# Kernel optimization log

Measured on AMD Instinct MI355X. Metric: run time of the kernel, lower is better.

The kernel has to match this reference:

```python
import jax, jax.numpy as jnp
import numpy as np

G = 17  # groups == deform_groups
EPS = 1e-5

# regular 3x3 kernel grid in homogeneous coords: rows = (dy, dx, 1), cols = 9 kernel taps (row-major)
REG = jnp.array([[-1, -1, -1, 0, 0, 0, 1, 1, 1],
                 [-1, 0, 1, -1, 0, 1, -1, 0, 1],
                 [1, 1, 1, 1, 1, 1, 1, 1, 1]], dtype=jnp.float32)
KY = jnp.array([-1, -1, -1, 0, 0, 0, 1, 1, 1], dtype=jnp.float32)
KX = jnp.array([-1, 0, 1, -1, 0, 1, -1, 0, 1], dtype=jnp.float32)


def setup_inputs() -> dict:
    key = jax.random.key(0)
    k0, k1, k2 = jax.random.split(key, 3)
    B, C, H, W = 2, 272, 128, 128
    Cg = C // G
    x = jax.random.normal(k0, (B, C, H, W), jnp.float32)
    tm_w = jax.random.normal(k1, (6 * G, Cg, 3, 3), jnp.float32) * 0.02  # offset-transform conv weight
    tm_b = jnp.zeros((6 * G,), jnp.float32)
    dc_w = jax.random.normal(k2, (C, Cg, 3, 3), jnp.float32) * 0.05     # deform conv weight (no bias)
    gamma = jnp.ones((C,), jnp.float32)
    beta = jnp.zeros((C,), jnp.float32)
    return dict(x=x, tm_w=tm_w, tm_b=tm_b, dc_w=dc_w, gamma=gamma, beta=beta)


def _deform_sample(x, dy, dx):
    """Bilinear-sample x (B,C,H,W) at per-group offsets dy,dx (B,H,W,G,9).
    Returns (B,G,Cg,9,H,W). Zero padding outside the image (mmcv semantics)."""
    B, C, H, W = x.shape
    Cg = C // G
    hh = jnp.arange(H, dtype=x.dtype)[None, :, None, None, None]
    ww = jnp.arange(W, dtype=x.dtype)[None, None, :, None, None]
    py = hh + KY + dy  # (B,H,W,G,9)
    px = ww + KX + dx
    y0 = jnp.floor(py)
    x0 = jnp.floor(px)
    wy = py - y0
    wx = px - x0
    y0i = y0.astype(jnp.int32)
    x0i = x0.astype(jnp.int32)
    x_g = x.reshape(B, G, Cg, H * W)

    def corner(yi, xi, wgt):
        valid = (yi >= 0) & (yi < H) & (xi >= 0) & (xi < W)
        lin = jnp.clip(yi, 0, H - 1) * W + jnp.clip(xi, 0, W - 1)  # (B,H,W,G,9)
        lin = lin.transpose(0, 3, 4, 1, 2).reshape(B, G, 1, 9 * H * W)
        idx = jnp.broadcast_to(lin, (B, G, Cg, 9 * H * W))
        vals = jnp.take_along_axis(x_g, idx, axis=3).reshape(B, G, Cg, 9, H, W)
        w = (wgt * valid.astype(x.dtype)).transpose(0, 3, 4, 1, 2)  # (B,G,9,H,W)
        return vals * w[:, :, None]

    samp = corner(y0i, x0i, (1 - wy) * (1 - wx))
    samp = samp + corner(y0i, x0i + 1, (1 - wy) * wx)
    samp = samp + corner(y0i + 1, x0i, wy * (1 - wx))
    samp = samp + corner(y0i + 1, x0i + 1, wy * wx)
    return samp


def _forward(x, tm_w, tm_b, dc_w, gamma, beta):
    B, C, H, W = x.shape
    Cg = C // G
    # 1) offset-transform conv (grouped 3x3, SAME)
    aff = jax.lax.conv_general_dilated(
        x, tm_w, window_strides=(1, 1), padding='SAME',
        dimension_numbers=('NCHW', 'OIHW', 'NCHW'), feature_group_count=G)
    aff = aff + tm_b[None, :, None, None]  # (B,6G,H,W)
    # faithful to torch: view(B,2,3,G,H,W).permute(0,4,5,3,1,2) @ REG
    aff = aff.reshape(B, 2, 3, G, H, W).transpose(0, 4, 5, 3, 1, 2)  # (B,H,W,G,2,3)
    off = jnp.einsum('bhwgij,jk->bhwgik', aff, REG)  # (B,H,W,G,2,9)
    # DeformConv2d reads the flattened 18 channels as interleaved (dy,dx) pairs per tap
    off = off.reshape(B, H, W, G, 18).reshape(B, H, W, G, 9, 2)
    dy, dx = off[..., 0], off[..., 1]
    # 2) deformable 3x3 conv, groups=deform_groups=G, bias=False
    samp = _deform_sample(x, dy, dx)  # (B,G,Cg,9,H,W)
    w = dc_w.reshape(G, Cg, Cg, 3 * 3)  # (g, out-in-group, in-in-group, tap)
    out = jnp.einsum('bgckhw,gock->bgohw', samp, w).reshape(B, C, H, W)
    # 3) batch norm (training-mode stats) + residual ReLU
    mean = jnp.mean(out, axis=(0, 2, 3), keepdims=True)
    var = jnp.var(out, axis=(0, 2, 3), keepdims=True)
    out = (out - mean) * jax.lax.rsqrt(var + EPS)
    out = out * gamma[None, :, None, None] + beta[None, :, None, None]
    return jax.nn.relu(out + x)


def reference(x, tm_w, tm_b, dc_w, gamma, beta):
    return _forward(x, tm_w, tm_b, dc_w, gamma, beta)
```

## Files before the change

### kernel.cpp

```cpp
#include <hip/hip_runtime.h>
#include <math.h>

#define BB 2
#define CC 272
#define GG 17
#define CG 16
#define HH 128
#define WW 128
#define HWX (HH*WW)
#define AFFC 102
#define NSLAB (BB*GG)
#define TILES_PER_SLAB 64
#define NWG (NSLAB*TILES_PER_SLAB)
#define WGPX (NWG/8)

typedef float f4nt __attribute__((ext_vector_type(4)));
typedef unsigned u4nt __attribute__((ext_vector_type(4)));

__device__ __forceinline__ unsigned f2bf(float f) {
    unsigned u = __float_as_uint(f);
    return (u + 0x7fffu + ((u >> 16) & 1u)) >> 16;
}
__device__ __forceinline__ float bflo(unsigned u) { return __uint_as_float(u << 16); }
__device__ __forceinline__ float bfhi(unsigned u) { return __uint_as_float(u & 0xffff0000u); }

__global__ __launch_bounds__(256) void wt_kernel(
    const float* __restrict__ dc_w, const float* __restrict__ tm_w,
    float* __restrict__ dc_wt, float* __restrict__ tm_wt)
{
    int i = blockIdx.x * 256 + threadIdx.x;
    if (i < GG * CG * 9 * CG) {
        int oc = i & 15, t = (i >> 4) % 9, c = (i / 144) % 16, g = i / 2304;
        dc_wt[i] = dc_w[((size_t)(g * 16 + oc) * 16 + c) * 9 + t];
    }
    if (i < GG * 6 * 9 * CG) {
        int c = i & 15, t = (i >> 4) % 9, j = (i / 144) % 6, ig = i / 864;
        tm_wt[i] = tm_w[((size_t)(ig * 6 + j) * 16 + c) * 9 + t];
    }
}

__global__ __launch_bounds__(256) void transpose_kernel(
    const float* __restrict__ x, unsigned* __restrict__ xt)
{
    __shared__ float tile[CG][WW + 1];
    const int h = blockIdx.x & (HH - 1);
    const int g = (blockIdx.x >> 7) % GG;
    const int b = blockIdx.x / (GG * HH);
    const int tid = threadIdx.x;
    const float* src = x + (size_t)(b * CC + g * CG) * HWX + h * WW;
    for (int i = tid; i < CG * WW; i += 256) {
        int c = i >> 7, w = i & (WW - 1);
        tile[c][w] = src[(size_t)c * HWX + w];
    }
    __syncthreads();
    unsigned* dst = xt + ((size_t)(b * GG + g) * HWX + h * WW) * (CG / 2);
    for (int i = tid; i < CG * WW / 2; i += 256) {
        int w = i >> 3, c2 = i & 7;
        dst[i] = f2bf(tile[2 * c2][w]) | (f2bf(tile[2 * c2 + 1][w]) << 16);
    }
}

__global__ __launch_bounds__(256) void aff_conv_kernel(
    const unsigned* __restrict__ xt, const float* __restrict__ tm_wt,
    const float* __restrict__ tm_b, float* __restrict__ aff)
{
    const int ig = blockIdx.y;
    const int b = blockIdx.z;
    const int tid = threadIdx.x;

    const int p = blockIdx.x * 256 + tid;
    const int h = p >> 7, w = p & (WW - 1);
    const unsigned* xb = xt + (size_t)(b * GG + ig) * HWX * (CG / 2);
    const float* wb = tm_wt + (size_t)ig * (6 * 9 * CG);

    float acc[6];
#pragma unroll
    for (int j = 0; j < 6; ++j) acc[j] = 0.f;

#pragma unroll 1
    for (int t = 0; t < 9; ++t) {
        int hy = h + t / 3 - 1;
        int wx = w + t % 3 - 1;
        uint4 u0 = {0, 0, 0, 0}, u1 = {0, 0, 0, 0};
        if (hy >= 0 && hy < HH && wx >= 0 && wx < WW) {
            const uint4* px = (const uint4*)(xb + (size_t)(hy * WW + wx) * (CG / 2));
            u0 = px[0]; u1 = px[1];
        }
        float xv[16];
        xv[0] = bflo(u0.x);  xv[1] = bfhi(u0.x);  xv[2] = bflo(u0.y);  xv[3] = bfhi(u0.y);
        xv[4] = bflo(u0.z);  xv[5] = bfhi(u0.z);  xv[6] = bflo(u0.w);  xv[7] = bfhi(u0.w);
        xv[8] = bflo(u1.x);  xv[9] = bfhi(u1.x);  xv[10] = bflo(u1.y); xv[11] = bfhi(u1.y);
        xv[12] = bflo(u1.z); xv[13] = bfhi(u1.z); xv[14] = bflo(u1.w); xv[15] = bfhi(u1.w);
#pragma unroll
        for (int j = 0; j < 6; ++j) {
            const float* wp = wb + (j * 9 + t) * CG;
            float a = acc[j];
#pragma unroll
            for (int k = 0; k < 16; ++k) a = fmaf(xv[k], wp[k], a);
            acc[j] = a;
        }
    }
#pragma unroll
    for (int j = 0; j < 6; ++j)
        aff[(size_t)(b * AFFC + ig * 6 + j) * HWX + p] = acc[j] + tm_b[ig * 6 + j];
}


#define ACCE(T, CH, S) { \
    const float4* wp_ = (const float4*)(wg + ((CH) * 9 + (T)) * CG); \
    float4 q0 = wp_[0], q1 = wp_[1], q2 = wp_[2], q3 = wp_[3]; \
    acc[0]  = fmaf(S, q0.x, acc[0]);  acc[1]  = fmaf(S, q0.y, acc[1]); \
    acc[2]  = fmaf(S, q0.z, acc[2]);  acc[3]  = fmaf(S, q0.w, acc[3]); \
    acc[4]  = fmaf(S, q1.x, acc[4]);  acc[5]  = fmaf(S, q1.y, acc[5]); \
    acc[6]  = fmaf(S, q1.z, acc[6]);  acc[7]  = fmaf(S, q1.w, acc[7]); \
    acc[8]  = fmaf(S, q2.x, acc[8]);  acc[9]  = fmaf(S, q2.y, acc[9]); \
    acc[10] = fmaf(S, q2.z, acc[10]); acc[11] = fmaf(S, q2.w, acc[11]); \
    acc[12] = fmaf(S, q3.x, acc[12]); acc[13] = fmaf(S, q3.y, acc[13]); \
    acc[14] = fmaf(S, q3.z, acc[14]); acc[15] = fmaf(S, q3.w, acc[15]); }

#define SE2(UA, UB, UC, UD, CH, T) { \
    float sl = fmaf(w00, bflo(UA), fmaf(w01, bflo(UB), fmaf(w10, bflo(UC), w11 * bflo(UD)))); \
    float sh = fmaf(w00, bfhi(UA), fmaf(w01, bfhi(UB), fmaf(w10, bfhi(UC), w11 * bfhi(UD)))); \
    ACCE(T, (CH), sl) ACCE(T, (CH) + 1, sh) }

#define TAP(T, I0, K0, I1, K1) { \
    float dy = ((I0) ? a10 : a00) * (float)((K0) / 3 - 1) \
             + ((I0) ? a11 : a01) * (float)((K0) % 3 - 1) + ((I0) ? a12 : a02); \
    float dx = ((I1) ? a10 : a00) * (float)((K1) / 3 - 1) \
             + ((I1) ? a11 : a01) * (float)((K1) % 3 - 1) + ((I1) ? a12 : a02); \
    float py = (float)(h + (T) / 3 - 1) + dy; \
    float px = (float)(w + (T) % 3 - 1) + dx; \
    float y0f = floorf(py), x0f = floorf(px); \
    float wy = py - y0f, wx = px - x0f; \
    int y0 = (int)y0f, x0 = (int)x0f; \
    int y1 = y0 + 1, x1 = x0 + 1; \
    bool vy0 = (y0 >= 0) && (y0 < HH), vy1 = (y1 >= 0) && (y1 < HH); \
    bool vx0 = (x0 >= 0) && (x0 < WW), vx1 = (x1 >= 0) && (x1 < WW); \
    int y0c = min(max(y0, 0), HH - 1), y1c = min(max(y1, 0), HH - 1); \
    int x0c = min(max(x0, 0), WW - 1), x1c = min(max(x1, 0), WW - 1); \
    float w00 = (vy0 && vx0) ? (1.f - wy) * (1.f - wx) : 0.f; \
    float w01 = (vy0 && vx1) ? (1.f - wy) * wx : 0.f; \
    float w10 = (vy1 && vx0) ? wy * (1.f - wx) : 0.f; \
    float w11 = (vy1 && vx1) ? wy * wx : 0.f; \
    const uint4* pA = (const uint4*)(xb + (size_t)(y0c * WW + x0c) * (CG / 2)); \
    const uint4* pB = (const uint4*)(xb + (size_t)(y0c * WW + x1c) * (CG / 2)); \
    const uint4* pC = (const uint4*)(xb + (size_t)(y1c * WW + x0c) * (CG / 2)); \
    const uint4* pD = (const uint4*)(xb + (size_t)(y1c * WW + x1c) * (CG / 2)); \
    uint4 A0 = pA[0], A1 = pA[1], B0 = pB[0], B1 = pB[1]; \
    uint4 C0 = pC[0], C1 = pC[1], D0 = pD[0], D1 = pD[1]; \
    SE2(A0.x, B0.x, C0.x, D0.x, 0, T)  SE2(A0.y, B0.y, C0.y, D0.y, 2, T) \
    SE2(A0.z, B0.z, C0.z, D0.z, 4, T)  SE2(A0.w, B0.w, C0.w, D0.w, 6, T) \
    SE2(A1.x, B1.x, C1.x, D1.x, 8, T)  SE2(A1.y, B1.y, C1.y, D1.y, 10, T) \
    SE2(A1.z, B1.z, C1.z, D1.z, 12, T) SE2(A1.w, B1.w, C1.w, D1.w, 14, T) }

__global__ __launch_bounds__(256, 6) void deform_kernel(
    const unsigned* __restrict__ xt, const float* __restrict__ dc_wt,
    const float* __restrict__ aff_buf, unsigned* __restrict__ pre,
    float* __restrict__ stat_sum, float* __restrict__ stat_sqs)
{
    __shared__ float red[CG][4][2];

    const int bid = blockIdx.x;
    const int work = (bid & 7) * WGPX + (bid >> 3);
    const int slab = work / TILES_PER_SLAB;
    const int tile = work % TILES_PER_SLAB;
    const int b = slab / GG;
    const int g = slab % GG;

    const int tid = threadIdx.y * 16 + threadIdx.x;
    const int h = (tile >> 3) * 16 + threadIdx.y;
    const int w = (tile & 7) * 16 + threadIdx.x;

    const float* ab = aff_buf + (size_t)b * AFFC * HWX + h * WW + w;
    float a00 = __builtin_nontemporal_load(ab + (size_t)(0 * 51 + 0 * 17 + g) * HWX);
    float a01 = __builtin_nontemporal_load(ab + (size_t)(0 * 51 + 1 * 17 + g) * HWX);
    float a02 = __builtin_nontemporal_load(ab + (size_t)(0 * 51 + 2 * 17 + g) * HWX);
    float a10 = __builtin_nontemporal_load(ab + (size_t)(1 * 51 + 0 * 17 + g) * HWX);
    float a11 = __builtin_nontemporal_load(ab + (size_t)(1 * 51 + 1 * 17 + g) * HWX);
    float a12 = __builtin_nontemporal_load(ab + (size_t)(1 * 51 + 2 * 17 + g) * HWX);

    const unsigned* xb = xt + (size_t)(b * GG + g) * HWX * (CG / 2);
    const float* wg = dc_wt + (size_t)g * (CG * 9 * CG);

    float acc[CG];
#pragma unroll
    for (int oc = 0; oc < CG; ++oc) acc[oc] = 0.f;

    TAP(0, 0, 0, 0, 1)
    TAP(1, 0, 2, 0, 3)
    TAP(2, 0, 4, 0, 5)
    TAP(3, 0, 6, 0, 7)
    TAP(4, 0, 8, 1, 0)
    TAP(5, 1, 1, 1, 2)
    TAP(6, 1, 3, 1, 4)
    TAP(7, 1, 5, 1, 6)
    TAP(8, 1, 7, 1, 8)

    unsigned pk[8];
#pragma unroll
    for (int k = 0; k < 8; ++k)
        pk[k] = f2bf(acc[2 * k]) | (f2bf(acc[2 * k + 1]) << 16);
    {
        u4nt q0 = {pk[0], pk[1], pk[2], pk[3]};
        u4nt q1 = {pk[4], pk[5], pk[6], pk[7]};
        u4nt* pp = (u4nt*)(pre + ((size_t)slab * HWX + h * WW + w) * (CG / 2));
        __builtin_nontemporal_store(q0, pp);
        __builtin_nontemporal_store(q1, pp + 1);
    }

    const int lane = tid & 63, wave = tid >> 6;
#pragma unroll
    for (int oc = 0; oc < CG; ++oc) {
        float s = acc[oc], q = acc[oc] * acc[oc];
#pragma unroll
        for (int off = 32; off > 0; off >>= 1) {
            s += __shfl_down(s, off);
            q += __shfl_down(q, off);
        }
        if (lane == 0) { red[oc][wave][0] = s; red[oc][wave][1] = q; }
    }
    __syncthreads();
    if (tid < CG) {
        float s = red[tid][0][0] + red[tid][1][0] + red[tid][2][0] + red[tid][3][0];
        float q = red[tid][0][1] + red[tid][1][1] + red[tid][2][1] + red[tid][3][1];
        int ch = g * CG + tid;
        atomicAdd(&stat_sum[ch], s);
        atomicAdd(&stat_sqs[ch], q);
    }
}

__global__ __launch_bounds__(256) void bn_res_relu_kernel(
    const unsigned* __restrict__ pre, const float* __restrict__ x,
    const float* __restrict__ ssum, const float* __restrict__ ssqs,
    const float* __restrict__ gamma, const float* __restrict__ beta,
    float* __restrict__ out)
{
    const int blk = blockIdx.x;
    const int slab = blk >> 4;
    const int chunk = blk & 15;
    const int b = slab / GG, g = slab % GG;
    const int px0 = chunk * 1024 + threadIdx.x * 4;

    const float n = (float)(BB * HWX);
    float sc[16], sh[16];
#pragma unroll
    for (int oc = 0; oc < 16; ++oc) {
        int ch = g * CG + oc;
        float mean = ssum[ch] / n;
        float var = ssqs[ch] / n - mean * mean;
        float s = rsqrtf(var + 1e-5f) * gamma[ch];
        sc[oc] = s;
        sh[oc] = fmaf(-mean, s, beta[ch]);
    }

    const uint4* pp = (const uint4*)(pre + ((size_t)slab * HWX + px0) * (CG / 2));
    unsigned Pu[32];
#pragma unroll
    for (int k = 0; k < 8; ++k) {
        uint4 v = pp[k];
        Pu[4 * k] = v.x; Pu[4 * k + 1] = v.y; Pu[4 * k + 2] = v.z; Pu[4 * k + 3] = v.w;
    }
    const float* xb = x + (size_t)(b * CC + g * CG) * HWX + px0;
    float* ob = out + (size_t)(b * CC + g * CG) * HWX + px0;

#pragma unroll
    for (int oc = 0; oc < 16; ++oc) {
        f4nt xv = __builtin_nontemporal_load((const f4nt*)(xb + (size_t)oc * HWX));
        f4nt r;
        float p0, p1, p2, p3;
        {
            unsigned u0 = Pu[0 * 8 + (oc >> 1)], u1 = Pu[1 * 8 + (oc >> 1)];
            unsigned u2 = Pu[2 * 8 + (oc >> 1)], u3 = Pu[3 * 8 + (oc >> 1)];
            p0 = (oc & 1) ? bfhi(u0) : bflo(u0);
            p1 = (oc & 1) ? bfhi(u1) : bflo(u1);
            p2 = (oc & 1) ? bfhi(u2) : bflo(u2);
            p3 = (oc & 1) ? bfhi(u3) : bflo(u3);
        }
        r.x = fmaxf(fmaf(p0, sc[oc], sh[oc]) + xv.x, 0.f);
        r.y = fmaxf(fmaf(p1, sc[oc], sh[oc]) + xv.y, 0.f);
        r.z = fmaxf(fmaf(p2, sc[oc], sh[oc]) + xv.z, 0.f);
        r.w = fmaxf(fmaf(p3, sc[oc], sh[oc]) + xv.w, 0.f);
        __builtin_nontemporal_store(r, (f4nt*)(ob + (size_t)oc * HWX));
    }
}

extern "C" void kernel_launch(void* const* d_in, const int* in_sizes, int n_in,
                              void* d_out, int out_size, void* d_ws, size_t ws_size,
                              hipStream_t stream)
{
    const float* x     = (const float*)d_in[0];
    const float* tm_w  = (const float*)d_in[1];
    const float* tm_b  = (const float*)d_in[2];
    const float* dc_w  = (const float*)d_in[3];
    const float* gamma = (const float*)d_in[4];
    const float* beta  = (const float*)d_in[5];
    float* out = (float*)d_out;

    float* ws = (float*)d_ws;
    float* stat_sum = ws;
    float* stat_sqs = ws + CC;
    float* dc_wt = ws + 2048;
    float* tm_wt = dc_wt + 39424;
    float* aff   = tm_wt + 14848;
    unsigned* xtb = (unsigned*)(aff + (size_t)BB * AFFC * HWX);
    unsigned* preb = xtb + (size_t)NSLAB * HWX * (CG / 2);

    (void)hipMemsetAsync(stat_sum, 0, 2 * CC * sizeof(float), stream);

    wt_kernel<<<dim3(153), dim3(256), 0, stream>>>(dc_w, tm_w, dc_wt, tm_wt);
    transpose_kernel<<<dim3(BB * GG * HH), dim3(256), 0, stream>>>(x, xtb);
    aff_conv_kernel<<<dim3(HWX / 256, GG, BB), dim3(256), 0, stream>>>(xtb, tm_wt, tm_b, aff);
    deform_kernel<<<dim3(NWG), dim3(16, 16), 0, stream>>>(
        xtb, dc_wt, aff, preb, stat_sum, stat_sqs);
    bn_res_relu_kernel<<<dim3(NSLAB * 16), dim3(256), 0, stream>>>(
        preb, x, stat_sum, stat_sqs, gamma, beta, out);
}
```

Measured before the change: 131.6 us.

## Switch bf16 activations/weights to fp16 packed math with fdot2 accumulation

Stores transposed activations and both weight tensors as packed fp16 pairs instead of bf16/fp32. Bilinear sampling becomes packed half2 arithmetic, and channel accumulation uses v_dot2 fp16 dot products into fp32, halving the FMA count and the weight load bytes in the deform and offset convs. The risk is fp16 range and precision loss in the interpolation (half-precision blend weights and sums) and in the offset conv feeding sampling positions.

```diff
diff --git a/kernel.cpp b/kernel.cpp
--- a/kernel.cpp
+++ b/kernel.cpp
@@ -16,6 +16,21 @@
 
 typedef float f4nt __attribute__((ext_vector_type(4)));
 typedef unsigned u4nt __attribute__((ext_vector_type(4)));
+typedef _Float16 h2 __attribute__((ext_vector_type(2)));
+
+__device__ __forceinline__ h2 bch(unsigned u) { return __builtin_bit_cast(h2, u); }
+__device__ __forceinline__ unsigned hpk(float a, float b) {
+    return __builtin_bit_cast(unsigned, __builtin_amdgcn_cvt_pkrtz(a, b));
+}
+__device__ __forceinline__ h2 hbc(float a) {
+    return __builtin_bit_cast(h2, __builtin_amdgcn_cvt_pkrtz(a, a));
+}
+
+#if __has_builtin(__builtin_amdgcn_fdot2)
+#define FDOT2(A, B, C) __builtin_amdgcn_fdot2((A), (B), (C), false)
+#else
+#define FDOT2(A, B, C) fmaf((float)(A).x, (float)(B).x, fmaf((float)(A).y, (float)(B).y, (C)))
+#endif
 
 __device__ __forceinline__ unsigned f2bf(float f) {
     unsigned u = __float_as_uint(f);
@@ -26,16 +41,20 @@
 
 __global__ __launch_bounds__(256) void wt_kernel(
     const float* __restrict__ dc_w, const float* __restrict__ tm_w,
-    float* __restrict__ dc_wt, float* __restrict__ tm_wt)
+    unsigned* __restrict__ dc_wh, unsigned* __restrict__ tm_wh)
 {
     int i = blockIdx.x * 256 + threadIdx.x;
-    if (i < GG * CG * 9 * CG) {
-        int oc = i & 15, t = (i >> 4) % 9, c = (i / 144) % 16, g = i / 2304;
-        dc_wt[i] = dc_w[((size_t)(g * 16 + oc) * 16 + c) * 9 + t];
-    }
-    if (i < GG * 6 * 9 * CG) {
-        int c = i & 15, t = (i >> 4) % 9, j = (i / 144) % 6, ig = i / 864;
-        tm_wt[i] = tm_w[((size_t)(ig * 6 + j) * 16 + c) * 9 + t];
+    if (i < GG * 8 * 9 * CG) {
+        int oc = i & 15, t = (i >> 4) % 9, cp = (i / 144) % 8, g = i / 1152;
+        float w0 = dc_w[((size_t)(g * 16 + oc) * 16 + 2 * cp) * 9 + t];
+        float w1 = dc_w[((size_t)(g * 16 + oc) * 16 + 2 * cp + 1) * 9 + t];
+        dc_wh[i] = hpk(w0, w1);
+    }
+    if (i < GG * 6 * 9 * 8) {
+        int cp = i & 7, t = (i >> 3) % 9, j = (i / 72) % 6, ig = i / 432;
+        float w0 = tm_w[((size_t)(ig * 6 + j) * 16 + 2 * cp) * 9 + t];
+        float w1 = tm_w[((size_t)(ig * 6 + j) * 16 + 2 * cp + 1) * 9 + t];
+        tm_wh[i] = hpk(w0, w1);
     }
 }
 
@@ -56,12 +75,12 @@
     unsigned* dst = xt + ((size_t)(b * GG + g) * HWX + h * WW) * (CG / 2);
     for (int i = tid; i < CG * WW / 2; i += 256) {
         int w = i >> 3, c2 = i & 7;
-        dst[i] = f2bf(tile[2 * c2][w]) | (f2bf(tile[2 * c2 + 1][w]) << 16);
+        dst[i] = hpk(tile[2 * c2][w], tile[2 * c2 + 1][w]);
     }
 }
 
 __global__ __launch_bounds__(256) void aff_conv_kernel(
-    const unsigned* __restrict__ xt, const float* __restrict__ tm_wt,
+    const unsigned* __restrict__ xt, const unsigned* __restrict__ tm_wh,
     const float* __restrict__ tm_b, float* __restrict__ aff)
 {
     const int ig = blockIdx.y;
@@ -71,7 +90,7 @@
     const int p = blockIdx.x * 256 + tid;
     const int h = p >> 7, w = p & (WW - 1);
     const unsigned* xb = xt + (size_t)(b * GG + ig) * HWX * (CG / 2);
-    const float* wb = tm_wt + (size_t)ig * (6 * 9 * CG);
+    const unsigned* wbh = tm_wh + (size_t)ig * (6 * 9 * 8);
 
     float acc[6];
 #pragma unroll
@@ -86,17 +105,15 @@
             const uint4* px = (const uint4*)(xb + (size_t)(hy * WW + wx) * (CG / 2));
             u0 = px[0]; u1 = px[1];
         }
-        float xv[16];
-        xv[0] = bflo(u0.x);  xv[1] = bfhi(u0.x);  xv[2] = bflo(u0.y);  xv[3] = bfhi(u0.y);
-        xv[4] = bflo(u0.z);  xv[5] = bfhi(u0.z);  xv[6] = bflo(u0.w);  xv[7] = bfhi(u0.w);
-        xv[8] = bflo(u1.x);  xv[9] = bfhi(u1.x);  xv[10] = bflo(u1.y); xv[11] = bfhi(u1.y);
-        xv[12] = bflo(u1.z); xv[13] = bfhi(u1.z); xv[14] = bflo(u1.w); xv[15] = bfhi(u1.w);
 #pragma unroll
         for (int j = 0; j < 6; ++j) {
-            const float* wp = wb + (j * 9 + t) * CG;
+            const uint4* wp = (const uint4*)(wbh + (j * 9 + t) * 8);
+            uint4 qa = wp[0], qb = wp[1];
             float a = acc[j];
-#pragma unroll
-            for (int k = 0; k < 16; ++k) a = fmaf(xv[k], wp[k], a);
+            a = FDOT2(bch(u0.x), bch(qa.x), a); a = FDOT2(bch(u0.y), bch(qa.y), a);
+            a = FDOT2(bch(u0.z), bch(qa.z), a); a = FDOT2(bch(u0.w), bch(qa.w), a);
+            a = FDOT2(bch(u1.x), bch(qb.x), a); a = FDOT2(bch(u1.y), bch(qb.y), a);
+            a = FDOT2(bch(u1.z), bch(qb.z), a); a = FDOT2(bch(u1.w), bch(qb.w), a);
             acc[j] = a;
         }
     }
@@ -106,22 +123,21 @@
 }
 
 
-#define ACCE(T, CH, S) { \
-    const float4* wp_ = (const float4*)(wg + ((CH) * 9 + (T)) * CG); \
-    float4 q0 = wp_[0], q1 = wp_[1], q2 = wp_[2], q3 = wp_[3]; \
-    acc[0]  = fmaf(S, q0.x, acc[0]);  acc[1]  = fmaf(S, q0.y, acc[1]); \
-    acc[2]  = fmaf(S, q0.z, acc[2]);  acc[3]  = fmaf(S, q0.w, acc[3]); \
-    acc[4]  = fmaf(S, q1.x, acc[4]);  acc[5]  = fmaf(S, q1.y, acc[5]); \
-    acc[6]  = fmaf(S, q1.z, acc[6]);  acc[7]  = fmaf(S, q1.w, acc[7]); \
-    acc[8]  = fmaf(S, q2.x, acc[8]);  acc[9]  = fmaf(S, q2.y, acc[9]); \
-    acc[10] = fmaf(S, q2.z, acc[10]); acc[11] = fmaf(S, q2.w, acc[11]); \
-    acc[12] = fmaf(S, q3.x, acc[12]); acc[13] = fmaf(S, q3.y, acc[13]); \
-    acc[14] = fmaf(S, q3.z, acc[14]); acc[15] = fmaf(S, q3.w, acc[15]); }
-
-#define SE2(UA, UB, UC, UD, CH, T) { \
-    float sl = fmaf(w00, bflo(UA), fmaf(w01, bflo(UB), fmaf(w10, bflo(UC), w11 * bflo(UD)))); \
-    float sh = fmaf(w00, bfhi(UA), fmaf(w01, bfhi(UB), fmaf(w10, bfhi(UC), w11 * bfhi(UD)))); \
-    ACCE(T, (CH), sl) ACCE(T, (CH) + 1, sh) }
+#define MACC(T, CP, S2) { \
+    const uint4* wp_ = (const uint4*)(wgh + ((CP) * 9 + (T)) * CG); \
+    uint4 q0 = wp_[0], q1 = wp_[1], q2 = wp_[2], q3 = wp_[3]; \
+    acc[0]  = FDOT2(S2, bch(q0.x), acc[0]);  acc[1]  = FDOT2(S2, bch(q0.y), acc[1]); \
+    acc[2]  = FDOT2(S2, bch(q0.z), acc[2]);  acc[3]  = FDOT2(S2, bch(q0.w), acc[3]); \
+    acc[4]  = FDOT2(S2, bch(q1.x), acc[4]);  acc[5]  = FDOT2(S2, bch(q1.y), acc[5]); \
+    acc[6]  = FDOT2(S2, bch(q1.z), acc[6]);  acc[7]  = FDOT2(S2, bch(q1.w), acc[7]); \
+    acc[8]  = FDOT2(S2, bch(q2.x), acc[8]);  acc[9]  = FDOT2(S2, bch(q2.y), acc[9]); \
+    acc[10] = FDOT2(S2, bch(q2.z), acc[10]); acc[11] = FDOT2(S2, bch(q2.w), acc[11]); \
+    acc[12] = FDOT2(S2, bch(q3.x), acc[12]); acc[13] = FDOT2(S2, bch(q3.y), acc[13]); \
+    acc[14] = FDOT2(S2, bch(q3.z), acc[14]); acc[15] = FDOT2(S2, bch(q3.w), acc[15]); }
+
+#define SEM(T, CP, UA, UB, UC, UD) { \
+    h2 s2 = bch(UA) * W00 + bch(UB) * W01 + bch(UC) * W10 + bch(UD) * W11; \
+    MACC(T, CP, s2) }
 
 #define TAP(T, I0, K0, I1, K1) { \
     float dy = ((I0) ? a10 : a00) * (float)((K0) / 3 - 1) \
@@ -142,19 +158,20 @@
     float w01 = (vy0 && vx1) ? (1.f - wy) * wx : 0.f; \
     float w10 = (vy1 && vx0) ? wy * (1.f - wx) : 0.f; \
     float w11 = (vy1 && vx1) ? wy * wx : 0.f; \
+    h2 W00 = hbc(w00), W01 = hbc(w01), W10 = hbc(w10), W11 = hbc(w11); \
     const uint4* pA = (const uint4*)(xb + (size_t)(y0c * WW + x0c) * (CG / 2)); \
     const uint4* pB = (const uint4*)(xb + (size_t)(y0c * WW + x1c) * (CG / 2)); \
     const uint4* pC = (const uint4*)(xb + (size_t)(y1c * WW + x0c) * (CG / 2)); \
     const uint4* pD = (const uint4*)(xb + (size_t)(y1c * WW + x1c) * (CG / 2)); \
     uint4 A0 = pA[0], A1 = pA[1], B0 = pB[0], B1 = pB[1]; \
     uint4 C0 = pC[0], C1 = pC[1], D0 = pD[0], D1 = pD[1]; \
-    SE2(A0.x, B0.x, C0.x, D0.x, 0, T)  SE2(A0.y, B0.y, C0.y, D0.y, 2, T) \
-    SE2(A0.z, B0.z, C0.z, D0.z, 4, T)  SE2(A0.w, B0.w, C0.w, D0.w, 6, T) \
-    SE2(A1.x, B1.x, C1.x, D1.x, 8, T)  SE2(A1.y, B1.y, C1.y, D1.y, 10, T) \
-    SE2(A1.z, B1.z, C1.z, D1.z, 12, T) SE2(A1.w, B1.w, C1.w, D1.w, 14, T) }
+    SEM(T, 0, A0.x, B0.x, C0.x, D0.x) SEM(T, 1, A0.y, B0.y, C0.y, D0.y) \
+    SEM(T, 2, A0.z, B0.z, C0.z, D0.z) SEM(T, 3, A0.w, B0.w, C0.w, D0.w) \
+    SEM(T, 4, A1.x, B1.x, C1.x, D1.x) SEM(T, 5, A1.y, B1.y, C1.y, D1.y) \
+    SEM(T, 6, A1.z, B1.z, C1.z, D1.z) SEM(T, 7, A1.w, B1.w, C1.w, D1.w) }
 
 __global__ __launch_bounds__(256, 6) void deform_kernel(
-    const unsigned* __restrict__ xt, const float* __restrict__ dc_wt,
+    const unsigned* __restrict__ xt, const unsigned* __restrict__ dc_wh,
     const float* __restrict__ aff_buf, unsigned* __restrict__ pre,
     float* __restrict__ stat_sum, float* __restrict__ stat_sqs)
 {
@@ -180,7 +197,7 @@
     float a12 = __builtin_nontemporal_load(ab + (size_t)(1 * 51 + 2 * 17 + g) * HWX);
 
     const unsigned* xb = xt + (size_t)(b * GG + g) * HWX * (CG / 2);
-    const float* wg = dc_wt + (size_t)g * (CG * 9 * CG);
+    const unsigned* wgh = dc_wh + (size_t)g * (8 * 9 * CG);
 
     float acc[CG];
 #pragma unroll
@@ -299,19 +316,19 @@
     float* ws = (float*)d_ws;
     float* stat_sum = ws;
     float* stat_sqs = ws + CC;
-    float* dc_wt = ws + 2048;
-    float* tm_wt = dc_wt + 39424;
-    float* aff   = tm_wt + 14848;
+    unsigned* dc_wh = (unsigned*)(ws + 2048);
+    unsigned* tm_wh = dc_wh + 19712;
+    float* aff = (float*)(tm_wh + 7424);
     unsigned* xtb = (unsigned*)(aff + (size_t)BB * AFFC * HWX);
     unsigned* preb = xtb + (size_t)NSLAB * HWX * (CG / 2);
 
     (void)hipMemsetAsync(stat_sum, 0, 2 * CC * sizeof(float), stream);
 
-    wt_kernel<<<dim3(153), dim3(256), 0, stream>>>(dc_w, tm_w, dc_wt, tm_wt);
+    wt_kernel<<<dim3(77), dim3(256), 0, stream>>>(dc_w, tm_w, dc_wh, tm_wh);
     transpose_kernel<<<dim3(BB * GG * HH), dim3(256), 0, stream>>>(x, xtb);
-    aff_conv_kernel<<<dim3(HWX / 256, GG, BB), dim3(256), 0, stream>>>(xtb, tm_wt, tm_b, aff);
+    aff_conv_kernel<<<dim3(HWX / 256, GG, BB), dim3(256), 0, stream>>>(xtb, tm_wh, tm_b, aff);
     deform_kernel<<<dim3(NWG), dim3(16, 16), 0, stream>>>(
-        xtb, dc_wt, aff, preb, stat_sum, stat_sqs);
+        xtb, dc_wh, aff, preb, stat_sum, stat_sqs);
     bn_res_relu_kernel<<<dim3(NSLAB * 16), dim3(256), 0, stream>>>(
         preb, x, stat_sum, stat_sqs, gamma, beta, out);
 }
```

After: 122.6 us. -6.9%, faster.
